# Performance work log

Measured on AMD Instinct MI355X. Metric: run time of the kernel, lower is better.

## Reference

```python
import jax, jax.numpy as jnp
import numpy as np

D_MODEL, D_K, D_V, H = 1024, 64, 64, 16
B, NQ, NK = 2, 2048, 2048


def setup_inputs() -> dict:
    key = jax.random.key(0)
    ks = jax.random.split(key, 12)
    hd = H * D_K
    xav = lambda k, shape: jax.random.uniform(k, shape, jnp.float32, -1.0, 1.0) * np.sqrt(6.0 / (shape[0] + shape[1]))
    return {
        "queries": jax.random.normal(ks[0], (B, NQ, D_MODEL), jnp.float32),
        "keys": jax.random.normal(ks[1], (B, NK, D_MODEL), jnp.float32),
        "values": jax.random.normal(ks[2], (B, NK, D_MODEL), jnp.float32),
        "memory": jax.random.uniform(ks[3], (B, NK), jnp.float32),
        "Wq": xav(ks[4], (D_MODEL, hd)), "bq": jnp.zeros((hd,), jnp.float32),
        "Wk": xav(ks[5], (D_MODEL, hd)), "bk": jnp.zeros((hd,), jnp.float32),
        "Wv": xav(ks[6], (D_MODEL, H * D_V)), "bv": jnp.zeros((H * D_V,), jnp.float32),
        "Wo": xav(ks[7], (H * D_V, D_MODEL)), "bo": jnp.zeros((D_MODEL,), jnp.float32),
        "Wmm": xav(ks[8], (1, H * D_V)), "bmm": jnp.zeros((H * D_V,), jnp.float32),
    }


def reference(queries, keys, values, memory, Wq, bq, Wk, bk, Wv, bv, Wo, bo, Wmm, bmm):
    b, nq = queries.shape[:2]
    nk = keys.shape[1]
    # projections -> (b, h, n, d)
    q = (queries @ Wq + bq).reshape(b, nq, H, D_K).transpose(0, 2, 1, 3)
    k = (keys @ Wk + bk).reshape(b, nk, H, D_K).transpose(0, 2, 1, 3)
    v = (values @ Wv + bv).reshape(b, nk, H, D_V).transpose(0, 2, 1, 3)
    # memory gate: fc_mm(memory[..., None]) -> (b, nk, h*d_k) -> (b, h, nk, d_k)
    mm = (memory[:, :, None] * Wmm[0] + bmm).reshape(b, nk, H, D_K).transpose(0, 2, 1, 3)
    att = jnp.einsum("bhqd,bhkd->bhqk", q, k * mm) / np.sqrt(D_K).astype(np.float32)
    att = jax.nn.softmax(att, axis=-1)
    out = jnp.einsum("bhqk,bhkd->bhqd", att, v * mm)
    out = out.transpose(0, 2, 1, 3).reshape(b, nq, H * D_V)
    return out @ Wo + bo
```

## Files before the change

kernel.cpp:

```cpp
#include <hip/hip_runtime.h>
#include <hip/hip_bf16.h>

#define H_   16
#define NQ_  2048
#define NK_  2048
#define DM_  1024

typedef float f32x4 __attribute__((ext_vector_type(4)));
typedef float f32x16 __attribute__((ext_vector_type(16)));
typedef __bf16 bf16x8 __attribute__((ext_vector_type(8)));
typedef unsigned short u16x8 __attribute__((ext_vector_type(8)));
typedef unsigned short u16x4 __attribute__((ext_vector_type(4)));

__device__ __forceinline__ unsigned short bfbits(float x) {
  __bf16 h = (__bf16)x;
  return __builtin_bit_cast(unsigned short, h);
}

__device__ __forceinline__ bf16x8 cvt8(float4 a, float4 b) {
  bf16x8 o;
  o[0] = (__bf16)a.x; o[1] = (__bf16)a.y; o[2] = (__bf16)a.z; o[3] = (__bf16)a.w;
  o[4] = (__bf16)b.x; o[5] = (__bf16)b.y; o[6] = (__bf16)b.z; o[7] = (__bf16)b.w;
  return o;
}

__global__ __launch_bounds__(256) void prep(
    const float* __restrict__ s0, const float* __restrict__ s1,
    const float* __restrict__ s2, const float* __restrict__ s3,
    unsigned short* __restrict__ d0, unsigned short* __restrict__ d1,
    unsigned short* __restrict__ d2, unsigned short* __restrict__ d3) {
  const float* src = (blockIdx.z == 0) ? s0 : (blockIdx.z == 1) ? s1 : (blockIdx.z == 2) ? s2 : s3;
  unsigned short* dst = (blockIdx.z == 0) ? d0 : (blockIdx.z == 1) ? d1 : (blockIdx.z == 2) ? d2 : d3;
  __shared__ float t[64][65];
  const int r0 = blockIdx.x * 64, c0 = blockIdx.y * 64;
  for (int i = threadIdx.x; i < 4096; i += 256) {
    int r = i >> 6, c = i & 63;
    t[r][c] = src[(size_t)(r0 + r) * DM_ + c0 + c];
  }
  __syncthreads();
  for (int i = threadIdx.x; i < 4096; i += 256) {
    int n = i >> 6, kk = i & 63;
    dst[(size_t)(c0 + n) * DM_ + r0 + kk] = bfbits(t[kk][n]);
  }
}

__device__ __forceinline__ void gll16(const unsigned short* g, unsigned short* l) {
  __builtin_amdgcn_global_load_lds((const __attribute__((address_space(1))) void*)g,
                                   (__attribute__((address_space(3))) void*)l, 16, 0, 0);
}

template <int MODE>
__device__ __forceinline__ void gemm128_body(
    int bx, int by,
    const void* __restrict__ Av, const void* __restrict__ Btv, int K,
    const float* __restrict__ bias, const float* __restrict__ mem,
    const float* __restrict__ Wmm, const float* __restrict__ bmm,
    unsigned short* __restrict__ obf,
    unsigned short* Al, unsigned short* Bl) {
  constexpr bool AF32 = (MODE <= 1);
  constexpr bool BF32 = (MODE == 2);
  const int tid = threadIdx.x, lane = tid & 63, w = tid >> 6;
  const int wm = w >> 1, wn = w & 1;
  const int m0 = bx * 128, n0 = by * 128;
  const int lrow = lane >> 2, lcol = (lane & 3) * 8;
  const int fr = lane & 15, fk = (lane >> 4) * 8;
  constexpr int TSZ = 128 * 32;

  f32x4 acc[4][4] = {};

  const size_t aoff = (size_t)(m0 + w * 32 + lrow) * K + lcol;
  const size_t boff = (size_t)(n0 + w * 32 + lrow) * K + lcol;
  const unsigned short* agb = (const unsigned short*)Av + aoff;
  const float*          agf = (const float*)Av + aoff;
  const unsigned short* bgb = (const unsigned short*)Btv + boff;
  const float*          bgf = (const float*)Btv + boff;
  const int os0 = (w * 32 + lrow) * 32 + lcol;
  const int os1 = (w * 32 + lrow + 16) * 32 + lcol;
  const int oa0 = (w * 32) * 32, oa1 = (w * 32 + 16) * 32;
  const size_t s16K = (size_t)16 * K;

  float4 fa0, fa1, fa2, fa3;
  float4 fb0, fb1, fb2, fb3;

  const int KT = K >> 5;
  if constexpr (AF32) {
    fa0 = *(const float4*)agf; fa1 = *(const float4*)(agf + 4);
    fa2 = *(const float4*)(agf + s16K); fa3 = *(const float4*)(agf + s16K + 4);
    *(bf16x8*)(Al + os0) = cvt8(fa0, fa1);
    *(bf16x8*)(Al + os1) = cvt8(fa2, fa3);
    agf += 32;
    fa0 = *(const float4*)agf; fa1 = *(const float4*)(agf + 4);
    fa2 = *(const float4*)(agf + s16K); fa3 = *(const float4*)(agf + s16K + 4);
    agf += 32;
  } else {
    gll16(agb, Al + oa0); gll16(agb + s16K, Al + oa1);
    agb += 32;
  }
  if constexpr (BF32) {
    fb0 = *(const float4*)bgf; fb1 = *(const float4*)(bgf + 4);
    fb2 = *(const float4*)(bgf + s16K); fb3 = *(const float4*)(bgf + s16K + 4);
    *(bf16x8*)(Bl + os0) = cvt8(fb0, fb1);
    *(bf16x8*)(Bl + os1) = cvt8(fb2, fb3);
    bgf += 32;
    fb0 = *(const float4*)bgf; fb1 = *(const float4*)(bgf + 4);
    fb2 = *(const float4*)(bgf + s16K); fb3 = *(const float4*)(bgf + s16K + 4);
    bgf += 32;
  } else {
    gll16(bgb, Bl + oa0); gll16(bgb + s16K, Bl + oa1);
    bgb += 32;
  }
  __syncthreads();

  for (int kt = 0; kt < KT; ++kt) {
    const int cb = (kt & 1) * TSZ;
    const int sb = TSZ - cb;
    if (kt + 1 < KT) {
      if constexpr (AF32) {
        *(bf16x8*)(Al + sb + os0) = cvt8(fa0, fa1);
        *(bf16x8*)(Al + sb + os1) = cvt8(fa2, fa3);
      } else {
        gll16(agb, Al + sb + oa0); gll16(agb + s16K, Al + sb + oa1);
        agb += 32;
      }
      if constexpr (BF32) {
        *(bf16x8*)(Bl + sb + os0) = cvt8(fb0, fb1);
        *(bf16x8*)(Bl + sb + os1) = cvt8(fb2, fb3);
      } else {
        gll16(bgb, Bl + sb + oa0); gll16(bgb + s16K, Bl + sb + oa1);
        bgb += 32;
      }
    }
    if (kt + 2 < KT) {
      if constexpr (AF32) {
        fa0 = *(const float4*)agf; fa1 = *(const float4*)(agf + 4);
        fa2 = *(const float4*)(agf + s16K); fa3 = *(const float4*)(agf + s16K + 4);
        agf += 32;
      }
      if constexpr (BF32) {
        fb0 = *(const float4*)bgf; fb1 = *(const float4*)(bgf + 4);
        fb2 = *(const float4*)(bgf + s16K); fb3 = *(const float4*)(bgf + s16K + 4);
        bgf += 32;
      }
    }
    bf16x8 af[4], bfr[4];
#pragma unroll
    for (int i = 0; i < 4; ++i)
      af[i] = *(const bf16x8*)&Al[cb + (wm * 64 + i * 16 + fr) * 32 + fk];
#pragma unroll
    for (int j = 0; j < 4; ++j)
      bfr[j] = *(const bf16x8*)&Bl[cb + (wn * 64 + j * 16 + fr) * 32 + fk];
#pragma unroll
    for (int i = 0; i < 4; ++i)
#pragma unroll
      for (int j = 0; j < 4; ++j)
        acc[i][j] = __builtin_amdgcn_mfma_f32_16x16x32_bf16(af[i], bfr[j], acc[i][j], 0, 0, 0);
    __syncthreads();
  }

#pragma unroll
  for (int i = 0; i < 4; ++i) {
    const int rowb = m0 + wm * 64 + i * 16 + (lane >> 4) * 4;
#pragma unroll
    for (int j = 0; j < 4; ++j) {
      const int col = n0 + wn * 64 + j * 16 + fr;
#pragma unroll
      for (int r = 0; r < 4; ++r) {
        float v = acc[i][j][r];
        int rr = rowb + r;
        if (MODE == 0) {
          int b = rr >> 11, nq = rr & 2047, h = col >> 6, d = col & 63;
          float val = (v + bias[col]) * 0.180336884f;
          obf[(((size_t)(b * H_ + h)) * NQ_ + nq) * 64 + d] = bfbits(val);
        } else if (MODE == 1) {
          int b = rr >> 11, nk = rr & 2047, h = col >> 6, d = col & 63;
          float gate = mem[b * NK_ + nk] * Wmm[col] + bmm[col];
          float val = (v + bias[col]) * gate;
          obf[(((size_t)(b * H_ + h)) * NK_ + nk) * 64 + d] = bfbits(val);
        } else {
          int b = col >> 11, key = col & 2047, h = rr >> 6, d = rr & 63;
          float gate = mem[b * NK_ + key] * Wmm[rr] + bmm[rr];
          float val = (v + bias[rr]) * gate;
          int keyp = (key & ~12) | ((key & 4) << 1) | ((key & 8) >> 1);
          obf[(((size_t)(b * H_ + h)) * 64 + d) * NK_ + keyp] = bfbits(val);
        }
      }
    }
  }
}

__global__ __launch_bounds__(256) void gemm_qkv3(
    const float* __restrict__ queries, const float* __restrict__ keys,
    const float* __restrict__ values, const unsigned short* __restrict__ WvT,
    const unsigned short* __restrict__ WqT, const unsigned short* __restrict__ WkT,
    const float* __restrict__ bq, const float* __restrict__ bk, const float* __restrict__ bv,
    const float* __restrict__ mem, const float* __restrict__ Wmm, const float* __restrict__ bmm,
    unsigned short* __restrict__ Qp, unsigned short* __restrict__ Kp,
    unsigned short* __restrict__ VpT) {
  __shared__ unsigned short Al[2 * 128 * 32];
  __shared__ unsigned short Bl[2 * 128 * 32];
  const int gid = (blockIdx.x & 7) * 96 + (blockIdx.x >> 3);
  if (gid < 256) {
    gemm128_body<0>(gid >> 3, gid & 7, queries, WqT, 1024, bq, nullptr, nullptr, nullptr,
                    Qp, Al, Bl);
  } else if (gid < 512) {
    int bb = gid - 256;
    gemm128_body<1>(bb >> 3, bb & 7, keys, WkT, 1024, bk, mem, Wmm, bmm, Kp, Al, Bl);
  } else {
    int bb = gid - 512;
    gemm128_body<2>(bb & 7, bb >> 3, WvT, values, 1024, bv, mem, Wmm, bmm, VpT, Al, Bl);
  }
}

__global__ __launch_bounds__(256) void gemm_out(
    const unsigned short* __restrict__ AO, const unsigned short* __restrict__ WoT,
    const float* __restrict__ bo, float* __restrict__ out) {
  __shared__ unsigned short Al[2 * 64 * 32];
  __shared__ unsigned short Bl[2 * 128 * 32];
  const int b = (blockIdx.x & 7) * 64 + (blockIdx.x >> 3);
  const int bx = b & 63, by = b >> 6;
  const int tid = threadIdx.x, lane = tid & 63, w = tid >> 6;
  const int wm = w >> 1, wn = w & 1;
  const int m0 = bx * 64, n0 = by * 128;
  const int lrow = lane >> 2, lcol = (lane & 3) * 8;
  const int fr = lane & 15, fk = (lane >> 4) * 8;
  const int K = 1024;
  constexpr int TA = 64 * 32, TB = 128 * 32;

  f32x4 acc[2][4] = {};

  const unsigned short* ag = AO + (size_t)(m0 + w * 16 + lrow) * K + lcol;
  const unsigned short* bg = WoT + (size_t)(n0 + w * 32 + lrow) * K + lcol;
  const int oa = (w * 16) * 32;
  const int ob0 = (w * 32) * 32, ob1 = (w * 32 + 16) * 32;
  const size_t s16K = (size_t)16 * K;

  gll16(ag, Al + oa);
  gll16(bg, Bl + ob0); gll16(bg + s16K, Bl + ob1);
  ag += 32; bg += 32;
  __syncthreads();

  for (int kt = 0; kt < 32; ++kt) {
    const int ca = (kt & 1) * TA, cbb = (kt & 1) * TB;
    const int sa = TA - ca, sbb = TB - cbb;
    if (kt + 1 < 32) {
      gll16(ag, Al + sa + oa);
      gll16(bg, Bl + sbb + ob0); gll16(bg + s16K, Bl + sbb + ob1);
      ag += 32; bg += 32;
    }
    bf16x8 af[2], bfr[4];
#pragma unroll
    for (int i = 0; i < 2; ++i)
      af[i] = *(const bf16x8*)&Al[ca + (wm * 32 + i * 16 + fr) * 32 + fk];
#pragma unroll
    for (int j = 0; j < 4; ++j)
      bfr[j] = *(const bf16x8*)&Bl[cbb + (wn * 64 + j * 16 + fr) * 32 + fk];
#pragma unroll
    for (int i = 0; i < 2; ++i)
#pragma unroll
      for (int j = 0; j < 4; ++j)
        acc[i][j] = __builtin_amdgcn_mfma_f32_16x16x32_bf16(af[i], bfr[j], acc[i][j], 0, 0, 0);
    __syncthreads();
  }

#pragma unroll
  for (int i = 0; i < 2; ++i) {
    const int rowb = m0 + wm * 32 + i * 16 + (lane >> 4) * 4;
#pragma unroll
    for (int j = 0; j < 4; ++j) {
      const int col = n0 + wn * 64 + j * 16 + fr;
#pragma unroll
      for (int r = 0; r < 4; ++r)
        out[(size_t)(rowb + r) * DM_ + col] = acc[i][j][r] + bo[col];
    }
  }
}

__global__ __launch_bounds__(256, 2) void flash_attn(const unsigned short* __restrict__ Qp,
                                                     const unsigned short* __restrict__ Kp,
                                                     const unsigned short* __restrict__ VpT,
                                                     unsigned short* __restrict__ AO) {
  __shared__ unsigned short Ks[2][128][66];
  __shared__ unsigned short Vs[2][64][130];

  const int tid = threadIdx.x, lane = tid & 63, w = tid >> 6;
  const int gid = (blockIdx.x & 7) * 64 + (blockIdx.x >> 3);
  const int bh = gid >> 4;
  const int qt = gid & 15;
  const int r31 = lane & 31, hi2 = lane >> 5;

  const unsigned short* qg = Qp + (((size_t)bh * NQ_) + qt * 128 + w * 32 + r31) * 64 + hi2 * 8;
  bf16x8 qf[4];
#pragma unroll
  for (int s = 0; s < 4; ++s) qf[s] = *(const bf16x8*)&qg[s * 16];

  const int krow = tid >> 1, kcol = (tid & 1) * 32;
  const int vrow = tid >> 2, vcol = (tid & 3) * 32;
  const unsigned short* kg = Kp + ((size_t)bh * NK_ + krow) * 64 + kcol;
  const unsigned short* vg = VpT + ((size_t)bh * 64 + vrow) * NK_ + vcol;

  f32x16 acc0 = {}, acc1 = {};
  float l_run = 0.0f;

  u16x8 kr[4], vr[4];
#pragma unroll
  for (int i = 0; i < 4; ++i) {
    kr[i] = *(const u16x8*)(kg + 8 * i);
    vr[i] = *(const u16x8*)(vg + 8 * i);
  }
#pragma unroll
  for (int i = 0; i < 4; ++i) {
    *(u16x8*)&Ks[0][krow][kcol + 8 * i] = kr[i];
    *(u16x8*)&Vs[0][vrow][vcol + 8 * i] = vr[i];
  }

  for (int kt = 0; kt < 16; ++kt) {
    const int cur = kt & 1;
    __syncthreads();

    if (kt + 1 < 16) {
      const unsigned short* kn = kg + (size_t)(kt + 1) * 128 * 64;
      const unsigned short* vn = vg + (kt + 1) * 128;
#pragma unroll
      for (int i = 0; i < 4; ++i) {
        kr[i] = *(const u16x8*)(kn + 8 * i);
        vr[i] = *(const u16x8*)(vn + 8 * i);
      }
    }

    f32x16 sv[4] = {};
    __builtin_amdgcn_s_setprio(1);
#pragma unroll
    for (int s = 0; s < 4; ++s) {
#pragma unroll
      for (int kb = 0; kb < 4; ++kb) {
        bf16x8 ka = *(const bf16x8*)&Ks[cur][kb * 32 + r31][s * 16 + hi2 * 8];
        sv[kb] = __builtin_amdgcn_mfma_f32_32x32x16_bf16(ka, qf[s], sv[kb], 0, 0, 0);
      }
    }
    __builtin_amdgcn_s_setprio(0);

    float psp[4] = {0.f, 0.f, 0.f, 0.f};
    bf16x8 pb[8];
#pragma unroll
    for (int kb = 0; kb < 4; ++kb) {
#pragma unroll
      for (int g = 0; g < 16; ++g) {
        float p = __builtin_amdgcn_exp2f(sv[kb][g]);
        psp[kb] += p;
        pb[2 * kb + (g >> 3)][g & 7] = (__bf16)p;
      }
    }
    float ps = (psp[0] + psp[1]) + (psp[2] + psp[3]);
    ps += __shfl_xor(ps, 32);
    l_run += ps;

    __builtin_amdgcn_s_setprio(1);
#pragma unroll
    for (int ks = 0; ks < 8; ++ks) {
      bf16x8 va0 = *(const bf16x8*)&Vs[cur][r31][ks * 16 + hi2 * 8];
      bf16x8 va1 = *(const bf16x8*)&Vs[cur][32 + r31][ks * 16 + hi2 * 8];
      acc0 = __builtin_amdgcn_mfma_f32_32x32x16_bf16(va0, pb[ks], acc0, 0, 0, 0);
      acc1 = __builtin_amdgcn_mfma_f32_32x32x16_bf16(va1, pb[ks], acc1, 0, 0, 0);
    }
    __builtin_amdgcn_s_setprio(0);

    if (kt + 1 < 16) {
#pragma unroll
      for (int i = 0; i < 4; ++i) {
        *(u16x8*)&Ks[cur ^ 1][krow][kcol + 8 * i] = kr[i];
        *(u16x8*)&Vs[cur ^ 1][vrow][vcol + 8 * i] = vr[i];
      }
    }
  }

  const int b = bh >> 4, h = bh & 15;
  const float linv = 1.0f / l_run;
  const int qrow = qt * 128 + w * 32 + r31;
  const size_t rowbase = (((size_t)b * NQ_ + qrow) << 10) + h * 64;
#pragma unroll
  for (int c = 0; c < 4; ++c) {
    u16x4 o0, o1;
#pragma unroll
    for (int i = 0; i < 4; ++i) {
      o0[i] = bfbits(acc0[c * 4 + i] * linv);
      o1[i] = bfbits(acc1[c * 4 + i] * linv);
    }
    *(u16x4*)&AO[rowbase + 8 * c + 4 * hi2]      = o0;
    *(u16x4*)&AO[rowbase + 32 + 8 * c + 4 * hi2] = o1;
  }
}

extern "C" void kernel_launch(void* const* d_in, const int* in_sizes, int n_in,
                              void* d_out, int out_size, void* d_ws, size_t ws_size,
                              hipStream_t stream) {
  const float* queries = (const float*)d_in[0];
  const float* keys    = (const float*)d_in[1];
  const float* values  = (const float*)d_in[2];
  const float* memory  = (const float*)d_in[3];
  const float* Wq  = (const float*)d_in[4];
  const float* bq  = (const float*)d_in[5];
  const float* Wk  = (const float*)d_in[6];
  const float* bk  = (const float*)d_in[7];
  const float* Wv  = (const float*)d_in[8];
  const float* bv  = (const float*)d_in[9];
  const float* Wo  = (const float*)d_in[10];
  const float* bo  = (const float*)d_in[11];
  const float* Wmm = (const float*)d_in[12];
  const float* bmm = (const float*)d_in[13];

  char* ws = (char*)d_ws;
  const size_t MB = 1024 * 1024;
  unsigned short* AO  = (unsigned short*)(ws);
  unsigned short* WqT = (unsigned short*)(ws + 8 * MB);
  unsigned short* WkT = (unsigned short*)(ws + 10 * MB);
  unsigned short* WvT = (unsigned short*)(ws + 12 * MB);
  unsigned short* WoT = (unsigned short*)(ws + 14 * MB);
  unsigned short* Qp  = (unsigned short*)(ws + 16 * MB);
  unsigned short* Kp  = (unsigned short*)(ws + 24 * MB);
  unsigned short* VpT = (unsigned short*)(ws + 32 * MB);

  prep<<<dim3(16, 16, 4), 256, 0, stream>>>(Wq, Wk, Wv, Wo, WqT, WkT, WvT, WoT);

  gemm_qkv3<<<768, 256, 0, stream>>>(queries, keys, values, WvT, WqT, WkT,
                                     bq, bk, bv, memory, Wmm, bmm, Qp, Kp, VpT);

  flash_attn<<<512, 256, 0, stream>>>(Qp, Kp, VpT, AO);

  gemm_out<<<512, 256, 0, stream>>>(AO, WoT, bo, (float*)d_out);
}
```

Measured before the change: 120.6 us.

## Load K/V tiles via direct global-to-LDS copies with XOR-swizzled layout

Replaces the register-staged K/V tile loads in the flash attention kernel with direct global-to-LDS loads (gll16), prefetching the next tile into the alternate buffer. The padded LDS layout is replaced by an unpadded layout with an XOR swizzle on 16-byte chunks to avoid bank conflicts. This frees VGPRs and removes the explicit LDS store phase, but relies on the swizzle matching between writer and reader, and on the barrier placement to guard the async writes.

```diff
diff --git a/kernel.cpp b/kernel.cpp
--- a/kernel.cpp
+++ b/kernel.cpp
@@ -279,51 +279,55 @@
                                                      const unsigned short* __restrict__ Kp,
                                                      const unsigned short* __restrict__ VpT,
                                                      unsigned short* __restrict__ AO) {
-  __shared__ unsigned short Ks[2][128][66];
-  __shared__ unsigned short Vs[2][64][130];
+  __shared__ unsigned short KsL[2][128 * 64];
+  __shared__ unsigned short VsL[2][64 * 128];
 
   const int tid = threadIdx.x, lane = tid & 63, w = tid >> 6;
   const int gid = (blockIdx.x & 7) * 64 + (blockIdx.x >> 3);
   const int bh = gid >> 4;
   const int qt = gid & 15;
-  const int r31 = lane & 31, hi2 = lane >> 5;
+  const int r31 = lane & 31, hi2 = lane >> 5, rx7 = lane & 7;
 
   const unsigned short* qg = Qp + (((size_t)bh * NQ_) + qt * 128 + w * 32 + r31) * 64 + hi2 * 8;
   bf16x8 qf[4];
 #pragma unroll
   for (int s = 0; s < 4; ++s) qf[s] = *(const bf16x8*)&qg[s * 16];
 
-  const int krow = tid >> 1, kcol = (tid & 1) * 32;
-  const int vrow = tid >> 2, vcol = (tid & 3) * 32;
-  const unsigned short* kg = Kp + ((size_t)bh * NK_ + krow) * 64 + kcol;
-  const unsigned short* vg = VpT + ((size_t)bh * 64 + vrow) * NK_ + vcol;
+  int koff[4], voff[8];
+#pragma unroll
+  for (int s = 0; s < 4; ++s) koff[s] = ((s * 2 + hi2) ^ rx7) * 8;
+#pragma unroll
+  for (int ks = 0; ks < 8; ++ks) voff[ks] = ((ks * 2 + hi2) ^ rx7) * 8;
+
+  const int kchunk = (lane & 7) ^ ((lane >> 3) & 7);
+  const unsigned short* kgB = Kp + (size_t)bh * NK_ * 64
+                              + (size_t)(w * 32 + (lane >> 3)) * 64 + kchunk * 8;
+  const int vce = (lane & 15) ^ (lane >> 4);
+  const int vco = (lane & 15) ^ (4 + (lane >> 4));
+  const unsigned short* vgB = VpT + (size_t)bh * 64 * NK_
+                              + (size_t)(w * 16 + (lane >> 4)) * NK_;
+
+#pragma unroll
+  for (int i = 0; i < 4; ++i) {
+    gll16(kgB + i * 512, &KsL[0][(w * 32 + i * 8) * 64]);
+    const int vc = (i & 1) ? vco : vce;
+    gll16(vgB + (size_t)i * 4 * NK_ + vc * 8, &VsL[0][(w * 16 + i * 4) * 128]);
+  }
+  __syncthreads();
 
   f32x16 acc0 = {}, acc1 = {};
   float l_run = 0.0f;
 
-  u16x8 kr[4], vr[4];
-#pragma unroll
-  for (int i = 0; i < 4; ++i) {
-    kr[i] = *(const u16x8*)(kg + 8 * i);
-    vr[i] = *(const u16x8*)(vg + 8 * i);
-  }
-#pragma unroll
-  for (int i = 0; i < 4; ++i) {
-    *(u16x8*)&Ks[0][krow][kcol + 8 * i] = kr[i];
-    *(u16x8*)&Vs[0][vrow][vcol + 8 * i] = vr[i];
-  }
-
   for (int kt = 0; kt < 16; ++kt) {
     const int cur = kt & 1;
-    __syncthreads();
-
     if (kt + 1 < 16) {
-      const unsigned short* kn = kg + (size_t)(kt + 1) * 128 * 64;
-      const unsigned short* vn = vg + (kt + 1) * 128;
+      const size_t ko = (size_t)(kt + 1) * 128 * 64;
+      const int vko = (kt + 1) * 128;
 #pragma unroll
       for (int i = 0; i < 4; ++i) {
-        kr[i] = *(const u16x8*)(kn + 8 * i);
-        vr[i] = *(const u16x8*)(vn + 8 * i);
+        gll16(kgB + ko + i * 512, &KsL[cur ^ 1][(w * 32 + i * 8) * 64]);
+        const int vc = (i & 1) ? vco : vce;
+        gll16(vgB + (size_t)i * 4 * NK_ + vko + vc * 8, &VsL[cur ^ 1][(w * 16 + i * 4) * 128]);
       }
     }
 
@@ -333,7 +337,7 @@
     for (int s = 0; s < 4; ++s) {
 #pragma unroll
       for (int kb = 0; kb < 4; ++kb) {
-        bf16x8 ka = *(const bf16x8*)&Ks[cur][kb * 32 + r31][s * 16 + hi2 * 8];
+        bf16x8 ka = *(const bf16x8*)&KsL[cur][(kb * 32 + r31) * 64 + koff[s]];
         sv[kb] = __builtin_amdgcn_mfma_f32_32x32x16_bf16(ka, qf[s], sv[kb], 0, 0, 0);
       }
     }
@@ -357,20 +361,14 @@
     __builtin_amdgcn_s_setprio(1);
 #pragma unroll
     for (int ks = 0; ks < 8; ++ks) {
-      bf16x8 va0 = *(const bf16x8*)&Vs[cur][r31][ks * 16 + hi2 * 8];
-      bf16x8 va1 = *(const bf16x8*)&Vs[cur][32 + r31][ks * 16 + hi2 * 8];
+      bf16x8 va0 = *(const bf16x8*)&VsL[cur][r31 * 128 + voff[ks]];
+      bf16x8 va1 = *(const bf16x8*)&VsL[cur][(32 + r31) * 128 + voff[ks]];
       acc0 = __builtin_amdgcn_mfma_f32_32x32x16_bf16(va0, pb[ks], acc0, 0, 0, 0);
       acc1 = __builtin_amdgcn_mfma_f32_32x32x16_bf16(va1, pb[ks], acc1, 0, 0, 0);
     }
     __builtin_amdgcn_s_setprio(0);
 
-    if (kt + 1 < 16) {
-#pragma unroll
-      for (int i = 0; i < 4; ++i) {
-        *(u16x8*)&Ks[cur ^ 1][krow][kcol + 8 * i] = kr[i];
-        *(u16x8*)&Vs[cur ^ 1][vrow][vcol + 8 * i] = vr[i];
-      }
-    }
+    __syncthreads();
   }
 
   const int b = bh >> 4, h = bh & 15;
```

Measured after the change: 119.5 us, median of 2. About the same (-0.9%).
